# Performance work log

Hardware: AMD Instinct MI355X
Metric: run time of the kernel (lower is better)

Reference implementation:

```python
import jax, jax.numpy as jnp
import numpy as np

H = 256          # hidden_channels
R = 64           # num_rbf
N = 20000        # nodes
E = 320000       # edges
CUTOFF_LO = 0.0
CUTOFF_UP = 5.0
LN_EPS = 1e-5


def _layernorm(x, g, b):
    mu = jnp.mean(x, axis=-1, keepdims=True)
    var = jnp.var(x, axis=-1, keepdims=True)
    return (x - mu) * jax.lax.rsqrt(var + LN_EPS) * g + b


def _cosine_cutoff(r):
    # cutoff_lower == 0 branch of CosineCutoff
    c = 0.5 * (jnp.cos(r * (jnp.pi / CUTOFF_UP)) + 1.0)
    return c * (r < CUTOFF_UP).astype(r.dtype)


def setup_inputs() -> dict:
    key = jax.random.key(0)
    ks = jax.random.split(key, 16)
    def xavier(k, shape):
        fan_in, fan_out = shape[1], shape[0]
        lim = np.sqrt(6.0 / (fan_in + fan_out))
        return jax.random.uniform(k, shape, jnp.float32, -lim, lim)
    x = jax.random.normal(ks[0], (N, H), jnp.float32)
    edge_index = jax.random.randint(ks[1], (2, E), 0, N, jnp.int64)
    edge_weight = jax.random.uniform(ks[2], (E,), jnp.float32, 0.0, CUTOFF_UP)
    edge_attr = jax.random.normal(ks[3], (E, R), jnp.float32)
    return {
        "x": x,
        "edge_index": edge_index,
        "edge_weight": edge_weight,
        "edge_attr": edge_attr,
        "ln_g": jnp.ones((H,), jnp.float32),
        "ln_b": jnp.zeros((H,), jnp.float32),
        "Wq": xavier(ks[4], (H, H)), "bq": jnp.zeros((H,), jnp.float32),
        "Wk": xavier(ks[5], (H, H)), "bk": jnp.zeros((H,), jnp.float32),
        "Wv": xavier(ks[6], (H, H)), "bv": jnp.zeros((H,), jnp.float32),
        "Wo": xavier(ks[7], (H, H)), "bo": jnp.zeros((H,), jnp.float32),
        "Wdk": xavier(ks[8], (H, R)), "bdk": jnp.zeros((H,), jnp.float32),
        "Wdv": xavier(ks[9], (H, R)), "bdv": jnp.zeros((H,), jnp.float32),
    }


def reference(x, edge_index, edge_weight, edge_attr,
              ln_g, ln_b, Wq, bq, Wk, bk, Wv, bv, Wo, bo, Wdk, bdk, Wdv, bdv):
    src = edge_index[0]  # j (messages come from)
    dst = edge_index[1]  # i (messages aggregate to)

    x_norm = _layernorm(x, ln_g, ln_b)                     # [N,H]
    q = x_norm @ Wq.T + bq                                 # [N,H]
    k = x_norm @ Wk.T + bk
    v = x_norm @ Wv.T + bv

    dk = jax.nn.silu(edge_attr @ Wdk.T + bdk)              # [E,H]
    dv = jax.nn.silu(edge_attr @ Wdv.T + bdv)              # [E,H]

    q_i = q[dst]                                           # [E,H]
    k_j = k[src]
    v_j = v[src]

    attn = jnp.sum(q_i * k_j * dk, axis=1)                 # [E]
    attn = jax.nn.silu(attn) * _cosine_cutoff(edge_weight) # [E]

    msg = v_j * dv * attn[:, None]                         # [E,H]
    agg = jax.ops.segment_sum(msg, dst, num_segments=x.shape[0])  # [N,H]

    out = agg @ Wo.T + bo
    return x + out
```

## Files before the change

kernel.cpp:

```cpp
#include <hip/hip_runtime.h>
#include <math.h>

#define NN 20000
#define H 256
#define R 64
#define EE 320000
#define LN_EPS 1e-5f
#define NB 79

using short8  = __attribute__((ext_vector_type(8))) short;
using ushort8 = __attribute__((ext_vector_type(8))) unsigned short;
using f32x4   = __attribute__((ext_vector_type(4))) float;

typedef __attribute__((address_space(3))) unsigned int lds_uint;
typedef const __attribute__((address_space(1))) unsigned int glb_uint;

__device__ __forceinline__ float silu_f(float x) {
    return x * __builtin_amdgcn_rcpf(1.0f + __expf(-x));
}

__device__ __forceinline__ unsigned short f2bf(float f) {
    unsigned u = __float_as_uint(f);
    u += 0x7fff + ((u >> 16) & 1);
    return (unsigned short)(u >> 16);
}
__device__ __forceinline__ float bf2f(unsigned short s) {
    return __uint_as_float(((unsigned)s) << 16);
}
__device__ __forceinline__ unsigned short f2h(float f) {
    unsigned r;
    asm("v_cvt_f16_f32 %0, %1" : "=v"(r) : "v"(f));
    return (unsigned short)r;
}
__device__ __forceinline__ float h2f(unsigned short h) {
    float f;
    asm("v_cvt_f32_f16 %0, %1" : "=v"(f) : "v"((unsigned)h));
    return f;
}

__device__ __forceinline__ int sw_idx(int row, int col) {
    return row * 64 + ((((col >> 3) ^ (row & 7)) << 3) | (col & 7));
}
__device__ __forceinline__ int dh_idx(int row, int col) {
    return row * 256 + (col ^ (((row >> 2) & 3) << 4));
}

__global__ __launch_bounds__(256) void k_prep(
    const float* __restrict__ Wq, const float* __restrict__ Wk,
    const float* __restrict__ Wv, const float* __restrict__ Wo,
    const float* __restrict__ g,  const float* __restrict__ b,
    const float* __restrict__ bq, const float* __restrict__ bk, const float* __restrict__ bv,
    const float* __restrict__ Wdk, const float* __restrict__ Wdv,
    unsigned short* __restrict__ wqkv_p, unsigned short* __restrict__ wo_p,
    unsigned short* __restrict__ wdk_p,  unsigned short* __restrict__ wdv_p,
    float* __restrict__ bias3, int* __restrict__ hist)
{
    const int bid = blockIdx.x, t = threadIdx.x;
    if (bid < 128) {
        const int mat = bid >> 5;
        const float* W = mat == 0 ? Wq : (mat == 1 ? Wk : (mat == 2 ? Wv : Wo));
        unsigned short* out = (mat < 3) ? wqkv_p + (size_t)mat * 131072 : wo_p;
        const int fold = mat < 3;
        const int flat = (bid & 31) * 256 + t;
        const int tile = flat >> 9;
        const int rem  = flat & 511;
        const int ks   = rem >> 6;
        const int lane = rem & 63;
        const int nl = lane & 15, quad = lane >> 4;
        const int h  = tile * 16 + nl;
        const int c0 = ks * 32 + quad * 8;
        short8 hi8, lo8;
        #pragma unroll
        for (int j = 0; j < 8; ++j) {
            float wv = W[(size_t)h * 256 + c0 + j];
            if (fold) wv *= g[c0 + j];
            const unsigned short hh = f2bf(wv);
            hi8[j] = (short)hh;
            lo8[j] = (short)f2bf(wv - bf2f(hh));
        }
        unsigned short* ob = out + ((size_t)(tile * 8 + ks)) * 1024;
        *(short8*)&ob[lane * 8] = hi8;
        *(short8*)&ob[512 + lane * 8] = lo8;
    } else if (bid < 160) {
        const int flat = (bid - 128) * 256 + t;
        const int mat  = flat >> 12;
        const int rem  = flat & 4095;
        const int hh   = rem >> 11;
        const int r2   = rem & 2047;
        const int row  = r2 >> 4;
        const int col4 = (r2 & 15) * 4;
        const float* W = mat == 0 ? Wdk : Wdv;
        unsigned short* out = (mat == 0 ? wdk_p : wdv_p) + hh * 16384;
        const float4 w4 = *(const float4*)(W + (size_t)(hh * 128 + row) * 64 + col4);
        const unsigned short h0 = f2bf(w4.x), h1 = f2bf(w4.y), h2 = f2bf(w4.z), h3 = f2bf(w4.w);
        ushort4 hi4 = {h0, h1, h2, h3};
        ushort4 lo4 = {f2bf(w4.x - bf2f(h0)), f2bf(w4.y - bf2f(h1)),
                       f2bf(w4.z - bf2f(h2)), f2bf(w4.w - bf2f(h3))};
        const int di = sw_idx(row, col4);
        *(ushort4*)&out[di] = hi4;
        *(ushort4*)&out[8192 + di] = lo4;
    } else if (bid < 163) {
        const int mat = bid - 160, h = t;
        const float* W  = mat == 0 ? Wq : (mat == 1 ? Wk : Wv);
        const float* bb = mat == 0 ? bq : (mat == 1 ? bk : bv);
        float s = 0.f;
        const float* wr = W + (size_t)h * 256;
        for (int c = 0; c < 256; c += 4) {
            const float4 w4 = *(const float4*)(wr + c);
            const float4 b4 = *(const float4*)(b + c);
            s += w4.x * b4.x + w4.y * b4.y + w4.z * b4.z + w4.w * b4.w;
        }
        bias3[mat * 256 + h] = bb[h] + s;
    } else {
        const int i = (bid - 163) * 256 + t;
        if (i < NN) hist[i] = 0;
    }
}

__global__ __launch_bounds__(64, 2) void k_ln_qkv(
    const float* __restrict__ x,
    const unsigned short* __restrict__ wqkv_p, const float* __restrict__ bias3,
    unsigned short* __restrict__ q, unsigned short* __restrict__ k,
    unsigned short* __restrict__ v)
{
    const int t = threadIdx.x;
    const int lane = t & 63;
    const int nl = lane & 15, quad = lane >> 4;
    const int nbase = blockIdx.x * 16;
    const int node = nbase + nl;
    const bool nv = node < NN;

    float xv[64];
    float sum = 0.f, sq = 0.f;
    {
        const float* xp = x + (size_t)node * H + quad * 8;
        #pragma unroll
        for (int ks = 0; ks < 8; ++ks) {
            float4 x0 = {0.f,0.f,0.f,0.f}, x1 = {0.f,0.f,0.f,0.f};
            if (nv) {
                x0 = *(const float4*)(xp + ks * 32);
                x1 = *(const float4*)(xp + ks * 32 + 4);
            }
            xv[ks*8+0]=x0.x; xv[ks*8+1]=x0.y; xv[ks*8+2]=x0.z; xv[ks*8+3]=x0.w;
            xv[ks*8+4]=x1.x; xv[ks*8+5]=x1.y; xv[ks*8+6]=x1.z; xv[ks*8+7]=x1.w;
            sum += x0.x+x0.y+x0.z+x0.w + x1.x+x1.y+x1.z+x1.w;
            sq  += x0.x*x0.x+x0.y*x0.y+x0.z*x0.z+x0.w*x0.w
                 + x1.x*x1.x+x1.y*x1.y+x1.z*x1.z+x1.w*x1.w;
        }
    }
    sum += __shfl_xor(sum, 16); sum += __shfl_xor(sum, 32);
    sq  += __shfl_xor(sq, 16);  sq  += __shfl_xor(sq, 32);
    const float mu  = sum * (1.0f / H);
    const float var = sq * (1.0f / H) - mu * mu;
    const float rs  = rsqrtf(var + LN_EPS);

    short8 a_hi[8], a_lo[8];
    #pragma unroll
    for (int ks = 0; ks < 8; ++ks) {
        #pragma unroll
        for (int j = 0; j < 8; ++j) {
            const float z = (xv[ks*8+j] - mu) * rs;
            const unsigned short hh = f2bf(z);
            a_hi[ks][j] = (short)hh;
            a_lo[ks][j] = (short)f2bf(z - bf2f(hh));
        }
    }

    for (int mat = 0; mat < 3; ++mat) {
        unsigned short* outp = mat == 0 ? q : (mat == 1 ? k : v);
        const float* bp = bias3 + mat * 256;
        const unsigned short* wb = wqkv_p + (size_t)mat * 131072 + lane * 8;
        for (int tile = 0; tile < 16; ++tile) {
            const unsigned short* gb = wb + (size_t)tile * 8192;
            const float bbv = bp[tile * 16 + nl];
            f32x4 acc = {bbv, bbv, bbv, bbv};
            #pragma unroll
            for (int ks = 0; ks < 8; ++ks) {
                const short8 b_hi = *(const short8*)(gb + ks * 1024);
                const short8 b_lo = *(const short8*)(gb + ks * 1024 + 512);
                acc = __builtin_amdgcn_mfma_f32_16x16x32_bf16(a_hi[ks], b_hi, acc, 0, 0, 0);
                acc = __builtin_amdgcn_mfma_f32_16x16x32_bf16(a_lo[ks], b_hi, acc, 0, 0, 0);
                acc = __builtin_amdgcn_mfma_f32_16x16x32_bf16(a_hi[ks], b_lo, acc, 0, 0, 0);
            }
            #pragma unroll
            for (int r = 0; r < 4; ++r) {
                const int onode = nbase + quad * 4 + r;
                if (onode < NN)
                    outp[(size_t)onode * H + tile * 16 + nl] = f2h(acc[r]);
            }
        }
    }
}

__global__ __launch_bounds__(256) void k_hist(const int* __restrict__ ei, int* __restrict__ hist) {
    int e = blockIdx.x * 256 + threadIdx.x;
    if (e < EE) atomicAdd(&hist[ei[EE + e]], 1);
}

__global__ __launch_bounds__(256) void k_scan1(const int* __restrict__ hist,
                                               int* __restrict__ cursor, int* __restrict__ bsum) {
    const int t = threadIdx.x, i = blockIdx.x * 256 + t;
    const int lane = t & 63, w = t >> 6;
    const int v = (i < NN) ? hist[i] : 0;
    int incl = v;
    #pragma unroll
    for (int off = 1; off < 64; off <<= 1) {
        int u = __shfl_up(incl, off);
        if (lane >= off) incl += u;
    }
    __shared__ int ws[4];
    if (lane == 63) ws[w] = incl;
    __syncthreads();
    int base = 0;
    #pragma unroll
    for (int j = 0; j < 4; ++j) if (j < w) base += ws[j];
    if (i < NN) cursor[i] = base + incl - v;
    if (t == 255) bsum[blockIdx.x] = base + incl;
}

__global__ __launch_bounds__(128) void k_scan2(int* __restrict__ bsum) {
    __shared__ int buf[128];
    const int t = threadIdx.x;
    const int v = (t < NB) ? bsum[t] : 0;
    buf[t] = v;
    __syncthreads();
    #pragma unroll
    for (int off = 1; off < 128; off <<= 1) {
        int add = (t >= off) ? buf[t - off] : 0;
        __syncthreads();
        buf[t] += add;
        __syncthreads();
    }
    if (t < NB) bsum[t] = buf[t] - v;
}

__global__ __launch_bounds__(256) void k_scatter(const int* __restrict__ ei,
                                                 const float* __restrict__ ew,
                                                 int* __restrict__ cursor,
                                                 const int* __restrict__ bsum,
                                                 int* __restrict__ perm,
                                                 int* __restrict__ srcs,
                                                 int* __restrict__ dsts,
                                                 float* __restrict__ ews) {
    int e = blockIdx.x * 256 + threadIdx.x;
    if (e < EE) {
        int s = ei[e];
        int d = ei[EE + e];
        int pos = atomicAdd(&cursor[d], 1) + bsum[d >> 8];
        perm[pos] = e;
        srcs[pos] = s;
        dsts[pos] = d;
        ews[pos] = ew[e];
    }
}

__global__ __launch_bounds__(256, 2) void k_edge(
    const unsigned short* __restrict__ q16, const unsigned short* __restrict__ k16,
    const unsigned short* __restrict__ v16,
    const float* __restrict__ ea,
    const unsigned short* __restrict__ wdk_p, const float* __restrict__ bdk,
    const unsigned short* __restrict__ wdv_p, const float* __restrict__ bdv,
    const int* __restrict__ perm, const int* __restrict__ srcs,
    const int* __restrict__ dsts, const float* __restrict__ ews,
    float* __restrict__ agg)
{
    __shared__ __align__(16) unsigned short w_region[2 * 128 * 64];
    __shared__ __align__(16) unsigned short dks_h[64 * 256];
    __shared__ float attn_s[64];
    __shared__ int src_s[64], dst_s[64];

    const unsigned short* w_hi_s = w_region;
    const unsigned short* w_lo_s = w_region + 128 * 64;

    const int t    = threadIdx.x;
    const int bi   = blockIdx.x;
    const int eb   = ((bi & 7) * 625 + (bi >> 3)) * 64;
    const int lane = t & 63, wave = t >> 6;
    const int nl   = lane & 15, quad = lane >> 4;
    const int estrip = wave * 16;
    const int tx = t & 31, ty = t >> 5;
    const int h0 = tx * 4, e0 = ty * 8;

    #define STAGE(PTR)                                                                \
    {                                                                                 \
        const ushort8* sp = (const ushort8*)(PTR) + t;                                \
        ushort8* dpw = (ushort8*)w_region + (t & 192);                                \
        _Pragma("unroll")                                                             \
        for (int c = 0; c < 8; ++c)                                                   \
            __builtin_amdgcn_global_load_lds((glb_uint*)(sp + c * 256),               \
                                             (lds_uint*)(dpw + c * 256), 16, 0, 0);   \
    }

    #define MFMA_TO_DKS(BIAS, HALF)                                                   \
    {                                                                                 \
        f32x4 accA[8];                                                                \
        _Pragma("unroll")                                                             \
        for (int tt = 0; tt < 8; ++tt) {                                              \
            const int wrow = tt * 16 + nl;                                            \
            short8 b_hi[2], b_lo[2];                                                  \
            _Pragma("unroll")                                                         \
            for (int ks = 0; ks < 2; ++ks) {                                          \
                const int idx = wrow * 64 + ((((ks * 4 + quad) ^ (nl & 7)) << 3));    \
                b_hi[ks] = *(const short8*)&w_hi_s[idx];                              \
                b_lo[ks] = *(const short8*)&w_lo_s[idx];                              \
            }                                                                         \
            const float bb = (BIAS)[(HALF) * 128 + tt * 16 + nl];                     \
            f32x4 acc = {bb, bb, bb, bb};                                             \
            _Pragma("unroll")                                                         \
            for (int ks = 0; ks < 2; ++ks) {                                          \
                acc = __builtin_amdgcn_mfma_f32_16x16x32_bf16(a_hi[ks], b_hi[ks], acc, 0, 0, 0); \
                acc = __builtin_amdgcn_mfma_f32_16x16x32_bf16(a_lo[ks], b_hi[ks], acc, 0, 0, 0); \
                acc = __builtin_amdgcn_mfma_f32_16x16x32_bf16(a_hi[ks], b_lo[ks], acc, 0, 0, 0); \
            }                                                                         \
            accA[tt] = acc;                                                           \
        }                                                                             \
        __syncthreads();                         \
        _Pragma("unroll")                                                             \
        for (int tt = 0; tt < 8; ++tt)                                                \
            _Pragma("unroll")                                                         \
            for (int r = 0; r < 4; ++r)                                               \
                dks_h[dh_idx(estrip + quad * 4 + r, (HALF) * 128 + tt * 16 + nl)] =   \
                    f2h(silu_f(accA[tt][r]));                                         \
    }

    STAGE(wdk_p);

    if (t < 64) {
        src_s[t] = srcs[eb + t];
        dst_s[t] = dsts[eb + t];
        attn_s[t] = 0.f;
    }

    short8 a_hi[2], a_lo[2];
    {
        const int e = perm[eb + estrip + nl];
        const float* ap = ea + (size_t)e * R + quad * 8;
        #pragma unroll
        for (int ks = 0; ks < 2; ++ks) {
            const f32x4 x0 = *(const f32x4*)(ap + ks * 32);
            const f32x4 x1 = *(const f32x4*)(ap + ks * 32 + 4);
            const float zz[8] = {x0[0], x0[1], x0[2], x0[3], x1[0], x1[1], x1[2], x1[3]};
            #pragma unroll
            for (int j = 0; j < 8; ++j) {
                const unsigned short hv = f2bf(zz[j]);
                a_hi[ks][j] = (short)hv;
                a_lo[ks][j] = (short)f2bf(zz[j] - bf2f(hv));
            }
        }
    }
    __syncthreads();

    {
        f32x4 accA[8];
        #pragma unroll
        for (int tt = 0; tt < 8; ++tt) {
            const int wrow = tt * 16 + nl;
            short8 b_hi[2], b_lo[2];
            #pragma unroll
            for (int ks = 0; ks < 2; ++ks) {
                const int idx = wrow * 64 + ((((ks * 4 + quad) ^ (nl & 7)) << 3));
                b_hi[ks] = *(const short8*)&w_hi_s[idx];
                b_lo[ks] = *(const short8*)&w_lo_s[idx];
            }
            const float bb = bdk[tt * 16 + nl];
            f32x4 acc = {bb, bb, bb, bb};
            #pragma unroll
            for (int ks = 0; ks < 2; ++ks) {
                acc = __builtin_amdgcn_mfma_f32_16x16x32_bf16(a_hi[ks], b_hi[ks], acc, 0, 0, 0);
                acc = __builtin_amdgcn_mfma_f32_16x16x32_bf16(a_lo[ks], b_hi[ks], acc, 0, 0, 0);
                acc = __builtin_amdgcn_mfma_f32_16x16x32_bf16(a_hi[ks], b_lo[ks], acc, 0, 0, 0);
            }
            accA[tt] = acc;
        }
        __syncthreads();
        STAGE(wdk_p + 16384);
        #pragma unroll
        for (int tt = 0; tt < 8; ++tt)
            #pragma unroll
            for (int r = 0; r < 4; ++r)
                dks_h[dh_idx(estrip + quad * 4 + r, tt * 16 + nl)] =
                    f2h(silu_f(accA[tt][r]));
    }
    __syncthreads();
    MFMA_TO_DKS(bdk, 1);
    STAGE(wdv_p);

    {
        float qv[8];
        int pd = -1;
        #pragma unroll
        for (int i = 0; i < 8; ++i) {
            const int d = dst_s[e0 + i], s = src_s[e0 + i];
            if (d != pd) {
                const ushort4 q0 = *(const ushort4*)(q16 + (size_t)d * H + h0);
                const ushort4 q1 = *(const ushort4*)(q16 + (size_t)d * H + 128 + h0);
                qv[0] = h2f(q0.x); qv[1] = h2f(q0.y); qv[2] = h2f(q0.z); qv[3] = h2f(q0.w);
                qv[4] = h2f(q1.x); qv[5] = h2f(q1.y); qv[6] = h2f(q1.z); qv[7] = h2f(q1.w);
                pd = d;
            }
            const ushort4 k0 = *(const ushort4*)(k16 + (size_t)s * H + h0);
            const ushort4 k1 = *(const ushort4*)(k16 + (size_t)s * H + 128 + h0);
            const ushort4 d40 = *(const ushort4*)&dks_h[dh_idx(e0 + i, h0)];
            const ushort4 d41 = *(const ushort4*)&dks_h[dh_idx(e0 + i, 128 + h0)];
            float part = qv[0] * h2f(k0.x) * h2f(d40.x) + qv[1] * h2f(k0.y) * h2f(d40.y)
                       + qv[2] * h2f(k0.z) * h2f(d40.z) + qv[3] * h2f(k0.w) * h2f(d40.w)
                       + qv[4] * h2f(k1.x) * h2f(d41.x) + qv[5] * h2f(k1.y) * h2f(d41.y)
                       + qv[6] * h2f(k1.z) * h2f(d41.z) + qv[7] * h2f(k1.w) * h2f(d41.w);
            #pragma unroll
            for (int off = 16; off; off >>= 1) part += __shfl_xor(part, off);
            if (tx == 0) attn_s[e0 + i] += part;
        }
    }
    __syncthreads();

    if (t < 64) {
        const float rr = ews[eb + t];
        const float cut = (rr < 5.0f) ? 0.5f * (__cosf(rr * 0.6283185307f) + 1.0f) : 0.0f;
        attn_s[t] = silu_f(attn_s[t]) * cut;
    }

    MFMA_TO_DKS(bdv, 0);
    STAGE(wdv_p + 16384);
    __syncthreads();
    MFMA_TO_DKS(bdv, 1);

    {
        float4 m0 = {0.f,0.f,0.f,0.f}, m1 = {0.f,0.f,0.f,0.f};
        int cur_d = -1;
        #pragma unroll
        for (int i = 0; i < 8; ++i) {
            const int d = dst_s[e0 + i], s = src_s[e0 + i];
            const float a = attn_s[e0 + i];
            const ushort4 v0 = *(const ushort4*)(v16 + (size_t)s * H + h0);
            const ushort4 v1 = *(const ushort4*)(v16 + (size_t)s * H + 128 + h0);
            const ushort4 d40 = *(const ushort4*)&dks_h[dh_idx(e0 + i, h0)];
            const ushort4 d41 = *(const ushort4*)&dks_h[dh_idx(e0 + i, 128 + h0)];
            const float w0x = h2f(v0.x) * h2f(d40.x) * a, w0y = h2f(v0.y) * h2f(d40.y) * a;
            const float w0z = h2f(v0.z) * h2f(d40.z) * a, w0w = h2f(v0.w) * h2f(d40.w) * a;
            const float w1x = h2f(v1.x) * h2f(d41.x) * a, w1y = h2f(v1.y) * h2f(d41.y) * a;
            const float w1z = h2f(v1.z) * h2f(d41.z) * a, w1w = h2f(v1.w) * h2f(d41.w) * a;
            if (d != cur_d) {
                if (cur_d >= 0) {
                    float* dp = agg + (size_t)cur_d * H;
                    atomicAdd(dp + h0 + 0, m0.x); atomicAdd(dp + h0 + 1, m0.y);
                    atomicAdd(dp + h0 + 2, m0.z); atomicAdd(dp + h0 + 3, m0.w);
                    atomicAdd(dp + 128 + h0 + 0, m1.x); atomicAdd(dp + 128 + h0 + 1, m1.y);
                    atomicAdd(dp + 128 + h0 + 2, m1.z); atomicAdd(dp + 128 + h0 + 3, m1.w);
                }
                m0.x = w0x; m0.y = w0y; m0.z = w0z; m0.w = w0w;
                m1.x = w1x; m1.y = w1y; m1.z = w1z; m1.w = w1w;
                cur_d = d;
            } else {
                m0.x += w0x; m0.y += w0y; m0.z += w0z; m0.w += w0w;
                m1.x += w1x; m1.y += w1y; m1.z += w1z; m1.w += w1w;
            }
        }
        {
            float* dp = agg + (size_t)cur_d * H;
            atomicAdd(dp + h0 + 0, m0.x); atomicAdd(dp + h0 + 1, m0.y);
            atomicAdd(dp + h0 + 2, m0.z); atomicAdd(dp + h0 + 3, m0.w);
            atomicAdd(dp + 128 + h0 + 0, m1.x); atomicAdd(dp + 128 + h0 + 1, m1.y);
            atomicAdd(dp + 128 + h0 + 2, m1.z); atomicAdd(dp + 128 + h0 + 3, m1.w);
        }
    }
    #undef MFMA_TO_DKS
    #undef STAGE
}

__global__ __launch_bounds__(64, 2) void k_out(
    const float* __restrict__ aggm, const unsigned short* __restrict__ wo_p,
    const float* __restrict__ bo, const float* __restrict__ x, float* __restrict__ out)
{
    const int t = threadIdx.x;
    const int lane = t & 63;
    const int nl = lane & 15, quad = lane >> 4;
    const int nbase = blockIdx.x * 16;
    const int node = nbase + nl;
    const bool nv = node < NN;

    short8 a_hi[8], a_lo[8];
    {
        const float* ap = aggm + (size_t)node * H + quad * 8;
        #pragma unroll
        for (int ks = 0; ks < 8; ++ks) {
            float4 x0 = {0.f,0.f,0.f,0.f}, x1 = {0.f,0.f,0.f,0.f};
            if (nv) { x0 = *(const float4*)(ap + ks * 32); x1 = *(const float4*)(ap + ks * 32 + 4); }
            const float zz[8] = {x0.x,x0.y,x0.z,x0.w,x1.x,x1.y,x1.z,x1.w};
            #pragma unroll
            for (int j = 0; j < 8; ++j) {
                const unsigned short hh = f2bf(zz[j]);
                a_hi[ks][j] = (short)hh;
                a_lo[ks][j] = (short)f2bf(zz[j] - bf2f(hh));
            }
        }
    }
    for (int tile = 0; tile < 16; ++tile) {
        const unsigned short* gb = wo_p + (size_t)tile * 8192 + lane * 8;
        const float bbv = bo[tile * 16 + nl];
        f32x4 acc = {bbv, bbv, bbv, bbv};
        #pragma unroll
        for (int ks = 0; ks < 8; ++ks) {
            const short8 b_hi = *(const short8*)(gb + ks * 1024);
            const short8 b_lo = *(const short8*)(gb + ks * 1024 + 512);
            acc = __builtin_amdgcn_mfma_f32_16x16x32_bf16(a_hi[ks], b_hi, acc, 0, 0, 0);
            acc = __builtin_amdgcn_mfma_f32_16x16x32_bf16(a_lo[ks], b_hi, acc, 0, 0, 0);
            acc = __builtin_amdgcn_mfma_f32_16x16x32_bf16(a_hi[ks], b_lo, acc, 0, 0, 0);
        }
        #pragma unroll
        for (int r = 0; r < 4; ++r) {
            const int onode = nbase + quad * 4 + r;
            if (onode < NN) {
                const size_t oi = (size_t)onode * H + tile * 16 + nl;
                out[oi] = x[oi] + acc[r];
            }
        }
    }
}

extern "C" void kernel_launch(void* const* d_in, const int* in_sizes, int n_in,
                              void* d_out, int out_size, void* d_ws, size_t ws_size,
                              hipStream_t stream) {
    const float* x   = (const float*)d_in[0];
    const int*   ei  = (const int*)d_in[1];
    const float* ew  = (const float*)d_in[2];
    const float* ea  = (const float*)d_in[3];
    const float* g   = (const float*)d_in[4];
    const float* b   = (const float*)d_in[5];
    const float* Wq  = (const float*)d_in[6];  const float* bq  = (const float*)d_in[7];
    const float* Wk  = (const float*)d_in[8];  const float* bk  = (const float*)d_in[9];
    const float* Wv  = (const float*)d_in[10]; const float* bv  = (const float*)d_in[11];
    const float* Wo  = (const float*)d_in[12]; const float* bo  = (const float*)d_in[13];
    const float* Wdk = (const float*)d_in[14]; const float* bdk = (const float*)d_in[15];
    const float* Wdv = (const float*)d_in[16]; const float* bdv = (const float*)d_in[17];

    unsigned short* q16 = (unsigned short*)d_ws;
    unsigned short* k16 = q16 + (size_t)NN * H;
    unsigned short* v16 = k16 + (size_t)NN * H;
    float* agg  = (float*)(v16 + (size_t)NN * H);
    int*   hist = (int*)(agg + (size_t)NN * H);
    int*   cur  = hist + NN;
    int*   bsum = cur + NN;
    int*   perm = bsum + 128;
    int*   srcs = perm + EE;
    int*   dsts = srcs + EE;
    float* ews  = (float*)(dsts + EE);
    unsigned short* wqkv_p = (unsigned short*)(ews + EE);
    unsigned short* wo_p   = wqkv_p + 393216;
    unsigned short* wdk_p  = wo_p + 131072;
    unsigned short* wdv_p  = wdk_p + 32768;
    float* bias3 = (float*)(wdv_p + 32768);

    hipMemsetAsync(agg, 0, (size_t)NN * H * sizeof(float), stream);
    k_prep<<<242, 256, 0, stream>>>(Wq, Wk, Wv, Wo, g, b, bq, bk, bv, Wdk, Wdv,
                                    wqkv_p, wo_p, wdk_p, wdv_p, bias3, hist);
    k_hist<<<EE / 256, 256, 0, stream>>>(ei, hist);
    k_ln_qkv<<<(NN + 15) / 16, 64, 0, stream>>>(x, wqkv_p, bias3, q16, k16, v16);
    k_scan1<<<NB, 256, 0, stream>>>(hist, cur, bsum);
    k_scan2<<<1, 128, 0, stream>>>(bsum);
    k_scatter<<<EE / 256, 256, 0, stream>>>(ei, ew, cur, bsum, perm, srcs, dsts, ews);
    k_edge<<<EE / 64, 256, 0, stream>>>(q16, k16, v16, ea, wdk_p, bdk, wdv_p, bdv,
                                        perm, srcs, dsts, ews, agg);
    k_out<<<(NN + 15) / 16, 64, 0, stream>>>(agg, wo_p, bo, x, (float*)d_out);
}
```

Baseline: 635.3 us.

## Make edge kernel wave-independent with fragment-packed weights read from global

The edge kernel stops staging the dk/dv weight matrices into shared memory through global_load_lds. Each wave now handles its own 16 edges with private shared buffers, so all block-level barriers are gone. The weights are pre-packed by the prep kernel into MFMA fragment order, letting each lane read its B fragments straight from global/L2 with one contiguous 16-byte load. Shared memory per block shrinks and the launch-bounds occupancy hint rises from 2 to 4 blocks. The cost is repeated weight reads from cache by every wave, plus possible register pressure under the higher occupancy target.

```diff
diff --git a/kernel.cpp b/kernel.cpp
--- a/kernel.cpp
+++ b/kernel.cpp
@@ -12,9 +12,6 @@
 using ushort8 = __attribute__((ext_vector_type(8))) unsigned short;
 using f32x4   = __attribute__((ext_vector_type(4))) float;
 
-typedef __attribute__((address_space(3))) unsigned int lds_uint;
-typedef const __attribute__((address_space(1))) unsigned int glb_uint;
-
 __device__ __forceinline__ float silu_f(float x) {
     return x * __builtin_amdgcn_rcpf(1.0f + __expf(-x));
 }
@@ -38,9 +35,6 @@
     return f;
 }
 
-__device__ __forceinline__ int sw_idx(int row, int col) {
-    return row * 64 + ((((col >> 3) ^ (row & 7)) << 3) | (col & 7));
-}
 __device__ __forceinline__ int dh_idx(int row, int col) {
     return row * 256 + (col ^ (((row >> 2) & 3) << 4));
 }
@@ -81,26 +75,35 @@
         unsigned short* ob = out + ((size_t)(tile * 8 + ks)) * 1024;
         *(short8*)&ob[lane * 8] = hi8;
         *(short8*)&ob[512 + lane * 8] = lo8;
-    } else if (bid < 160) {
+    } else if (bid < 144) {
         const int flat = (bid - 128) * 256 + t;
-        const int mat  = flat >> 12;
-        const int rem  = flat & 4095;
-        const int hh   = rem >> 11;
-        const int r2   = rem & 2047;
-        const int row  = r2 >> 4;
-        const int col4 = (r2 & 15) * 4;
+        const int mat  = flat >> 11;
+        const int rem  = flat & 2047;
+        const int hh   = rem >> 10;
+        const int r2   = rem & 1023;
+        const int tile = r2 >> 7;
+        const int r3   = r2 & 127;
+        const int ks   = r3 >> 6;
+        const int lane = r3 & 63;
+        const int nl = lane & 15, quad = lane >> 4;
         const float* W = mat == 0 ? Wdk : Wdv;
-        unsigned short* out = (mat == 0 ? wdk_p : wdv_p) + hh * 16384;
-        const float4 w4 = *(const float4*)(W + (size_t)(hh * 128 + row) * 64 + col4);
-        const unsigned short h0 = f2bf(w4.x), h1 = f2bf(w4.y), h2 = f2bf(w4.z), h3 = f2bf(w4.w);
-        ushort4 hi4 = {h0, h1, h2, h3};
-        ushort4 lo4 = {f2bf(w4.x - bf2f(h0)), f2bf(w4.y - bf2f(h1)),
-                       f2bf(w4.z - bf2f(h2)), f2bf(w4.w - bf2f(h3))};
-        const int di = sw_idx(row, col4);
-        *(ushort4*)&out[di] = hi4;
-        *(ushort4*)&out[8192 + di] = lo4;
-    } else if (bid < 163) {
-        const int mat = bid - 160, h = t;
+        unsigned short* out = (mat == 0 ? wdk_p : wdv_p)
+                            + hh * 16384 + (tile * 2 + ks) * 1024 + lane * 8;
+        const float* wr = W + (size_t)(hh * 128 + tile * 16 + nl) * 64 + ks * 32 + quad * 8;
+        const float4 w0 = *(const float4*)wr;
+        const float4 w1 = *(const float4*)(wr + 4);
+        const float zz[8] = {w0.x, w0.y, w0.z, w0.w, w1.x, w1.y, w1.z, w1.w};
+        short8 hi8, lo8;
+        #pragma unroll
+        for (int j = 0; j < 8; ++j) {
+            const unsigned short hv = f2bf(zz[j]);
+            hi8[j] = (short)hv;
+            lo8[j] = (short)f2bf(zz[j] - bf2f(hv));
+        }
+        *(short8*)out = hi8;
+        *(short8*)(out + 512) = lo8;
+    } else if (bid < 147) {
+        const int mat = bid - 144, h = t;
         const float* W  = mat == 0 ? Wq : (mat == 1 ? Wk : Wv);
         const float* bb = mat == 0 ? bq : (mat == 1 ? bk : bv);
         float s = 0.f;
@@ -112,7 +115,7 @@
         }
         bias3[mat * 256 + h] = bb[h] + s;
     } else {
-        const int i = (bid - 163) * 256 + t;
+        const int i = (bid - 147) * 256 + t;
         if (i < NN) hist[i] = 0;
     }
 }
@@ -254,7 +257,7 @@
     }
 }
 
-__global__ __launch_bounds__(256, 2) void k_edge(
+__global__ __launch_bounds__(256, 4) void k_edge(
     const unsigned short* __restrict__ q16, const unsigned short* __restrict__ k16,
     const unsigned short* __restrict__ v16,
     const float* __restrict__ ea,
@@ -264,45 +267,59 @@
     const int* __restrict__ dsts, const float* __restrict__ ews,
     float* __restrict__ agg)
 {
-    __shared__ __align__(16) unsigned short w_region[2 * 128 * 64];
-    __shared__ __align__(16) unsigned short dks_h[64 * 256];
-    __shared__ float attn_s[64];
-    __shared__ int src_s[64], dst_s[64];
-
-    const unsigned short* w_hi_s = w_region;
-    const unsigned short* w_lo_s = w_region + 128 * 64;
+    __shared__ __align__(16) unsigned short dks_all[4 * 16 * 256];
+    __shared__ int   srcw_all[4 * 16], dstw_all[4 * 16];
+    __shared__ float attw_all[4 * 16];
 
     const int t    = threadIdx.x;
     const int bi   = blockIdx.x;
-    const int eb   = ((bi & 7) * 625 + (bi >> 3)) * 64;
-    const int lane = t & 63, wave = t >> 6;
-    const int nl   = lane & 15, quad = lane >> 4;
-    const int estrip = wave * 16;
-    const int tx = t & 31, ty = t >> 5;
-    const int h0 = tx * 4, e0 = ty * 8;
-
-    #define STAGE(PTR)                                                                \
+    const int wave = t >> 6, lane = t & 63;
+    const int eb2  = (((bi & 7) * 625 + (bi >> 3)) * 4 + wave) * 16;
+
+    unsigned short* dksw = dks_all + wave * 4096;
+    int*   srcw = srcw_all + wave * 16;
+    int*   dstw = dstw_all + wave * 16;
+    float* attw = attw_all + wave * 16;
+
+    const int nl = lane & 15, quad = lane >> 4;
+    const int tx = lane & 31, ty2 = lane >> 5;
+    const int h0 = tx * 4, e0l = ty2 * 8;
+
+    if (lane < 16) {
+        srcw[lane] = srcs[eb2 + lane];
+        dstw[lane] = dsts[eb2 + lane];
+    }
+
+    short8 a_hi[2], a_lo[2];
+    {
+        const int e = perm[eb2 + nl];
+        const float* ap = ea + (size_t)e * R + quad * 8;
+        #pragma unroll
+        for (int ks = 0; ks < 2; ++ks) {
+            const f32x4 x0 = *(const f32x4*)(ap + ks * 32);
+            const f32x4 x1 = *(const f32x4*)(ap + ks * 32 + 4);
+            const float zz[8] = {x0[0], x0[1], x0[2], x0[3], x1[0], x1[1], x1[2], x1[3]};
+            #pragma unroll
+            for (int j = 0; j < 8; ++j) {
+                const unsigned short hv = f2bf(zz[j]);
+                a_hi[ks][j] = (short)hv;
+                a_lo[ks][j] = (short)f2bf(zz[j] - bf2f(hv));
+            }
+        }
+    }
+
+    #define MFMA_DKS(IMG, BIAS, HALF)                                                 \
     {                                                                                 \
-        const ushort8* sp = (const ushort8*)(PTR) + t;                                \
-        ushort8* dpw = (ushort8*)w_region + (t & 192);                                \
-        _Pragma("unroll")                                                             \
-        for (int c = 0; c < 8; ++c)                                                   \
-            __builtin_amdgcn_global_load_lds((glb_uint*)(sp + c * 256),               \
-                                             (lds_uint*)(dpw + c * 256), 16, 0, 0);   \
-    }
-
-    #define MFMA_TO_DKS(BIAS, HALF)                                                   \
-    {                                                                                 \
+        const unsigned short* img_ = (IMG);                                           \
         f32x4 accA[8];                                                                \
         _Pragma("unroll")                                                             \
         for (int tt = 0; tt < 8; ++tt) {                                              \
-            const int wrow = tt * 16 + nl;                                            \
             short8 b_hi[2], b_lo[2];                                                  \
             _Pragma("unroll")                                                         \
             for (int ks = 0; ks < 2; ++ks) {                                          \
-                const int idx = wrow * 64 + ((((ks * 4 + quad) ^ (nl & 7)) << 3));    \
-                b_hi[ks] = *(const short8*)&w_hi_s[idx];                              \
-                b_lo[ks] = *(const short8*)&w_lo_s[idx];                              \
+                const unsigned short* fb = img_ + (tt * 2 + ks) * 1024 + lane * 8;    \
+                b_hi[ks] = *(const short8*)fb;                                        \
+                b_lo[ks] = *(const short8*)(fb + 512);                                \
             }                                                                         \
             const float bb = (BIAS)[(HALF) * 128 + tt * 16 + nl];                     \
             f32x4 acc = {bb, bb, bb, bb};                                             \
@@ -314,83 +331,23 @@
             }                                                                         \
             accA[tt] = acc;                                                           \
         }                                                                             \
-        __syncthreads();                         \
         _Pragma("unroll")                                                             \
         for (int tt = 0; tt < 8; ++tt)                                                \
             _Pragma("unroll")                                                         \
             for (int r = 0; r < 4; ++r)                                               \
-                dks_h[dh_idx(estrip + quad * 4 + r, (HALF) * 128 + tt * 16 + nl)] =   \
+                dksw[dh_idx(quad * 4 + r, (HALF) * 128 + tt * 16 + nl)] =             \
                     f2h(silu_f(accA[tt][r]));                                         \
     }
 
-    STAGE(wdk_p);
-
-    if (t < 64) {
-        src_s[t] = srcs[eb + t];
-        dst_s[t] = dsts[eb + t];
-        attn_s[t] = 0.f;
-    }
-
-    short8 a_hi[2], a_lo[2];
-    {
-        const int e = perm[eb + estrip + nl];
-        const float* ap = ea + (size_t)e * R + quad * 8;
-        #pragma unroll
-        for (int ks = 0; ks < 2; ++ks) {
-            const f32x4 x0 = *(const f32x4*)(ap + ks * 32);
-            const f32x4 x1 = *(const f32x4*)(ap + ks * 32 + 4);
-            const float zz[8] = {x0[0], x0[1], x0[2], x0[3], x1[0], x1[1], x1[2], x1[3]};
-            #pragma unroll
-            for (int j = 0; j < 8; ++j) {
-                const unsigned short hv = f2bf(zz[j]);
-                a_hi[ks][j] = (short)hv;
-                a_lo[ks][j] = (short)f2bf(zz[j] - bf2f(hv));
-            }
-        }
-    }
-    __syncthreads();
-
-    {
-        f32x4 accA[8];
-        #pragma unroll
-        for (int tt = 0; tt < 8; ++tt) {
-            const int wrow = tt * 16 + nl;
-            short8 b_hi[2], b_lo[2];
-            #pragma unroll
-            for (int ks = 0; ks < 2; ++ks) {
-                const int idx = wrow * 64 + ((((ks * 4 + quad) ^ (nl & 7)) << 3));
-                b_hi[ks] = *(const short8*)&w_hi_s[idx];
-                b_lo[ks] = *(const short8*)&w_lo_s[idx];
-            }
-            const float bb = bdk[tt * 16 + nl];
-            f32x4 acc = {bb, bb, bb, bb};
-            #pragma unroll
-            for (int ks = 0; ks < 2; ++ks) {
-                acc = __builtin_amdgcn_mfma_f32_16x16x32_bf16(a_hi[ks], b_hi[ks], acc, 0, 0, 0);
-                acc = __builtin_amdgcn_mfma_f32_16x16x32_bf16(a_lo[ks], b_hi[ks], acc, 0, 0, 0);
-                acc = __builtin_amdgcn_mfma_f32_16x16x32_bf16(a_hi[ks], b_lo[ks], acc, 0, 0, 0);
-            }
-            accA[tt] = acc;
-        }
-        __syncthreads();
-        STAGE(wdk_p + 16384);
-        #pragma unroll
-        for (int tt = 0; tt < 8; ++tt)
-            #pragma unroll
-            for (int r = 0; r < 4; ++r)
-                dks_h[dh_idx(estrip + quad * 4 + r, tt * 16 + nl)] =
-                    f2h(silu_f(accA[tt][r]));
-    }
-    __syncthreads();
-    MFMA_TO_DKS(bdk, 1);
-    STAGE(wdv_p);
+    MFMA_DKS(wdk_p,         bdk, 0);
+    MFMA_DKS(wdk_p + 16384, bdk, 1);
 
     {
         float qv[8];
         int pd = -1;
         #pragma unroll
         for (int i = 0; i < 8; ++i) {
-            const int d = dst_s[e0 + i], s = src_s[e0 + i];
+            const int d = dstw[e0l + i], s = srcw[e0l + i];
             if (d != pd) {
                 const ushort4 q0 = *(const ushort4*)(q16 + (size_t)d * H + h0);
                 const ushort4 q1 = *(const ushort4*)(q16 + (size_t)d * H + 128 + h0);
@@ -400,41 +357,38 @@
             }
             const ushort4 k0 = *(const ushort4*)(k16 + (size_t)s * H + h0);
             const ushort4 k1 = *(const ushort4*)(k16 + (size_t)s * H + 128 + h0);
-            const ushort4 d40 = *(const ushort4*)&dks_h[dh_idx(e0 + i, h0)];
-            const ushort4 d41 = *(const ushort4*)&dks_h[dh_idx(e0 + i, 128 + h0)];
+            const ushort4 d40 = *(const ushort4*)&dksw[dh_idx(e0l + i, h0)];
+            const ushort4 d41 = *(const ushort4*)&dksw[dh_idx(e0l + i, 128 + h0)];
             float part = qv[0] * h2f(k0.x) * h2f(d40.x) + qv[1] * h2f(k0.y) * h2f(d40.y)
                        + qv[2] * h2f(k0.z) * h2f(d40.z) + qv[3] * h2f(k0.w) * h2f(d40.w)
                        + qv[4] * h2f(k1.x) * h2f(d41.x) + qv[5] * h2f(k1.y) * h2f(d41.y)
                        + qv[6] * h2f(k1.z) * h2f(d41.z) + qv[7] * h2f(k1.w) * h2f(d41.w);
             #pragma unroll
             for (int off = 16; off; off >>= 1) part += __shfl_xor(part, off);
-            if (tx == 0) attn_s[e0 + i] += part;
-        }
-    }
-    __syncthreads();
-
-    if (t < 64) {
-        const float rr = ews[eb + t];
+            if (tx == 0) attw[e0l + i] = part;
+        }
+    }
+
+    if (lane < 16) {
+        const float rr = ews[eb2 + lane];
         const float cut = (rr < 5.0f) ? 0.5f * (__cosf(rr * 0.6283185307f) + 1.0f) : 0.0f;
-        attn_s[t] = silu_f(attn_s[t]) * cut;
-    }
-
-    MFMA_TO_DKS(bdv, 0);
-    STAGE(wdv_p + 16384);
-    __syncthreads();
-    MFMA_TO_DKS(bdv, 1);
+        attw[lane] = silu_f(attw[lane]) * cut;
+    }
+
+    MFMA_DKS(wdv_p,         bdv, 0);
+    MFMA_DKS(wdv_p + 16384, bdv, 1);
 
     {
         float4 m0 = {0.f,0.f,0.f,0.f}, m1 = {0.f,0.f,0.f,0.f};
         int cur_d = -1;
         #pragma unroll
         for (int i = 0; i < 8; ++i) {
-            const int d = dst_s[e0 + i], s = src_s[e0 + i];
-            const float a = attn_s[e0 + i];
+            const int d = dstw[e0l + i], s = srcw[e0l + i];
+            const float a = attw[e0l + i];
             const ushort4 v0 = *(const ushort4*)(v16 + (size_t)s * H + h0);
             const ushort4 v1 = *(const ushort4*)(v16 + (size_t)s * H + 128 + h0);
-            const ushort4 d40 = *(const ushort4*)&dks_h[dh_idx(e0 + i, h0)];
-            const ushort4 d41 = *(const ushort4*)&dks_h[dh_idx(e0 + i, 128 + h0)];
+            const ushort4 d40 = *(const ushort4*)&dksw[dh_idx(e0l + i, h0)];
+            const ushort4 d41 = *(const ushort4*)&dksw[dh_idx(e0l + i, 128 + h0)];
             const float w0x = h2f(v0.x) * h2f(d40.x) * a, w0y = h2f(v0.y) * h2f(d40.y) * a;
             const float w0z = h2f(v0.z) * h2f(d40.z) * a, w0w = h2f(v0.w) * h2f(d40.w) * a;
             const float w1x = h2f(v1.x) * h2f(d41.x) * a, w1y = h2f(v1.y) * h2f(d41.y) * a;
@@ -463,8 +417,7 @@
             atomicAdd(dp + 128 + h0 + 2, m1.z); atomicAdd(dp + 128 + h0 + 3, m1.w);
         }
     }
-    #undef MFMA_TO_DKS
-    #undef STAGE
+    #undef MFMA_DKS
 }
 
 __global__ __launch_bounds__(64, 2) void k_out(
@@ -551,7 +504,7 @@
     float* bias3 = (float*)(wdv_p + 32768);
 
     hipMemsetAsync(agg, 0, (size_t)NN * H * sizeof(float), stream);
-    k_prep<<<242, 256, 0, stream>>>(Wq, Wk, Wv, Wo, g, b, bq, bk, bv, Wdk, Wdv,
+    k_prep<<<226, 256, 0, stream>>>(Wq, Wk, Wv, Wo, g, b, bq, bk, bv, Wdk, Wdv,
                                     wqkv_p, wo_p, wdk_p, wdv_p, bias3, hist);
     k_hist<<<EE / 256, 256, 0, stream>>>(ei, hist);
     k_ln_qkv<<<(NN + 15) / 16, 64, 0, stream>>>(x, wqkv_p, bias3, q16, k16, v16);
```

Result: no change. 628.0 us (-1.1%).
